# Optimization experiments

Measured on AMD Instinct MI355X. Metric: run time of the kernel, lower is better.

Reference implementation:

```python
import jax, jax.numpy as jnp
import numpy as np

N, E = 50000, 400000
F, P = 20, 8          # NUM_FREQ, NUM_POWER_CLASS (edge/node attn dim)
D, H = 128, 8         # d_model, heads
C = D // H            # head dim
FF, L = 512, 2        # dim_feedforward, num layers
EPS = 1e-5


def setup_inputs() -> dict:
    key = jax.random.key(0)
    ks = jax.random.split(key, 24)
    g = lambda k, s: jax.random.normal(k, s, dtype=jnp.float32) * 0.02
    return {
        "freq_alloc": jax.random.normal(ks[0], (N, F), jnp.float32),
        "node_power_attn": jax.random.normal(ks[1], (N, P), jnp.float32),
        "edge_power_attn": jax.random.normal(ks[2], (E, P), jnp.float32),
        "edge_index": jax.random.randint(ks[3], (2, E), 0, N),
        "ptr": jnp.sort(jax.random.randint(ks[4], (65,), 0, N)),
        # GraphTransformer input/embedding projections
        "W_in": g(ks[5], (F, D)), "b_in": jnp.zeros((D,), jnp.float32),
        "W_emb": g(ks[6], (P, D)), "b_emb": jnp.zeros((D,), jnp.float32),
        # per-layer TransformerConv params (stacked over L)
        "Wq": g(ks[7], (L, D, D)), "bq": jnp.zeros((L, D), jnp.float32),
        "Wk": g(ks[8], (L, D, D)), "bk": jnp.zeros((L, D), jnp.float32),
        "Wv": g(ks[9], (L, D, D)), "bv": jnp.zeros((L, D), jnp.float32),
        "We": g(ks[10], (L, P, D)),                      # lin_edge, bias=False
        "Wskip": g(ks[11], (L, D, D)), "bskip": jnp.zeros((L, D), jnp.float32),
        # per-layer FFN + LayerNorms
        "W1": g(ks[12], (L, D, FF)), "b1": jnp.zeros((L, FF), jnp.float32),
        "W2": g(ks[13], (L, FF, D)), "b2": jnp.zeros((L, D), jnp.float32),
        "ln1_g": jnp.ones((L, D), jnp.float32), "ln1_b": jnp.zeros((L, D), jnp.float32),
        "ln2_g": jnp.ones((L, D), jnp.float32), "ln2_b": jnp.zeros((L, D), jnp.float32),
        # output head
        "W_out": g(ks[14], (D, F)), "b_out": jnp.zeros((F,), jnp.float32),
    }


def _ln(x, g, b):
    mu = jnp.mean(x, axis=-1, keepdims=True)
    var = jnp.mean(jnp.square(x - mu), axis=-1, keepdims=True)
    return (x - mu) * jax.lax.rsqrt(var + EPS) * g + b


def reference(freq_alloc, node_power_attn, edge_power_attn, edge_index, ptr,
              W_in, b_in, W_emb, b_emb,
              Wq, bq, Wk, bk, Wv, bv, We, Wskip, bskip,
              W1, b1, W2, b2, ln1_g, ln1_b, ln2_g, ln2_b,
              W_out, b_out):
    # dropout layers are identity (inference / dropout=0)
    src, dst = edge_index[0], edge_index[1]  # PyG: messages flow src -> dst
    inp = freq_alloc @ W_in + b_in           # [N, D]
    x = node_power_attn @ W_emb + b_emb      # [N, D]
    scale = jnp.float32(1.0 / np.sqrt(C))
    for l in range(L):
        x = x + inp
        # --- TransformerConv (heads concat, root_weight=True, beta=False) ---
        q = (x @ Wq[l] + bq[l]).reshape(N, H, C)
        k = (x @ Wk[l] + bk[l]).reshape(N, H, C)
        v = (x @ Wv[l] + bv[l]).reshape(N, H, C)
        e = (edge_power_attn @ We[l]).reshape(E, H, C)   # edge embedding
        kj = k[src] + e                                   # [E, H, C]
        alpha = jnp.einsum('ehc,ehc->eh', q[dst], kj) * scale  # [E, H]
        # segment softmax over incoming edges of each dst node
        m = jnp.full((N, H), -jnp.inf, alpha.dtype).at[dst].max(alpha)
        ex = jnp.exp(alpha - m[dst])
        s = jnp.zeros((N, H), alpha.dtype).at[dst].add(ex)
        a = ex / s[dst]                                   # [E, H]
        msg = (v[src] + e) * a[:, :, None]                # [E, H, C]
        agg = jnp.zeros((N, H, C), x.dtype).at[dst].add(msg).reshape(N, D)
        x2 = agg + x @ Wskip[l] + bskip[l]
        # --- residual + norm + FFN + norm ---
        x = _ln(x + x2, ln1_g[l], ln1_b[l])
        x2 = jax.nn.relu(x @ W1[l] + b1[l]) @ W2[l] + b2[l]
        x = _ln(x + x2, ln2_g[l], ln2_b[l])
    logit = x @ W_out + b_out                             # [N, F]
    unallocated = jnp.sum(freq_alloc, axis=1, keepdims=True) < 1.0
    return jnp.where(unallocated, logit, -jnp.inf)
```

## Files before the change

### kernel.cpp

```cpp
#include <hip/hip_runtime.h>
#include <cstdint>
#include <cstddef>

typedef unsigned int uint;
typedef unsigned short ushort;
typedef unsigned char uchar;
typedef __attribute__((ext_vector_type(8))) short bf16x8;
typedef __attribute__((ext_vector_type(8))) ushort u16x8;
typedef __attribute__((ext_vector_type(4))) float f32x4;
typedef __attribute__((ext_vector_type(2))) float f32x2;
typedef __attribute__((ext_vector_type(2))) _Float16 h2v;

__device__ __forceinline__ ushort f2bf(float x) {
    uint u = __float_as_uint(x);
    u += 0x7fffu + ((u >> 16) & 1u);
    return (ushort)(u >> 16);
}
__device__ __forceinline__ float bflo(uint w) { return __uint_as_float(w << 16); }
__device__ __forceinline__ float bfhi(uint w) { return __uint_as_float(w & 0xffff0000u); }
__device__ __forceinline__ float bf1(ushort u) { return __uint_as_float(((uint)u) << 16); }
__device__ __forceinline__ uint pack2(float a, float b) { return (uint)f2bf(a) | ((uint)f2bf(b) << 16); }
__device__ __forceinline__ uint pack2h(float a, float b) {
    union { _Float16 h[2]; uint u; } c;
    c.h[0] = (_Float16)a; c.h[1] = (_Float16)b; return c.u;
}
__device__ __forceinline__ h2v ash2(uint u) { union { uint u; h2v h; } c; c.u = u; return c.h; }

__device__ __forceinline__ uchar enc8_sw(float x) {
    uint u = __float_as_uint(x);
    uint s = (u >> 31) << 7;
    float a = fabsf(x);
    if (a > 448.f) return (uchar)(s | 0x7E);
    if (a < 0.001953125f) return (uchar)s;
    int e; float m = frexpf(a, &e);
    int E = e - 1 + 7;
    if (E <= 0) {
        int qi = (int)(a * 512.f + 0.5f);
        if (qi > 7) qi = 7;
        return (uchar)(s | qi);
    }
    int M = (int)((m * 2.f - 1.f) * 8.f + 0.5f);
    if (M == 8) { M = 0; E++; }
    if (E > 15) return (uchar)(s | 0x7E);
    return (uchar)(s | (E << 3) | M);
}
__device__ __forceinline__ float dec8_sw(uint b) {
    int s = (b >> 7) & 1, E = (b >> 3) & 15, M = b & 7;
    float v = E ? ldexpf(1.f + M * 0.125f, E - 7) : ldexpf((float)M * 0.125f, -6);
    return s ? -v : v;
}
__device__ __forceinline__ uint pk8(float a, float b, float c, float d) {
#if __has_builtin(__builtin_amdgcn_cvt_pk_fp8_f32)
    int w = __builtin_amdgcn_cvt_pk_fp8_f32(a, b, 0, false);
    w = __builtin_amdgcn_cvt_pk_fp8_f32(c, d, w, true);
    return (uint)w;
#else
    return (uint)enc8_sw(a) | ((uint)enc8_sw(b) << 8) | ((uint)enc8_sw(c) << 16) | ((uint)enc8_sw(d) << 24);
#endif
}
__device__ __forceinline__ void dec4(uint w, float* o) {
#if __has_builtin(__builtin_amdgcn_cvt_pk_f32_fp8)
    f32x2 lo = __builtin_amdgcn_cvt_pk_f32_fp8(w, false);
    f32x2 hi = __builtin_amdgcn_cvt_pk_f32_fp8(w, true);
    o[0] = lo[0]; o[1] = lo[1]; o[2] = hi[0]; o[3] = hi[1];
#else
    o[0] = dec8_sw(w & 255); o[1] = dec8_sw((w >> 8) & 255);
    o[2] = dec8_sw((w >> 16) & 255); o[3] = dec8_sw((w >> 24) & 255);
#endif
}


__global__ __launch_bounds__(256) void k_zero_i(int* __restrict__ p, int n) {
    int i = blockIdx.x * 256 + threadIdx.x;
    if (i < n) p[i] = 0;
}

__global__ __launch_bounds__(256) void k_count(const int* __restrict__ dst, int* __restrict__ cnt, int n) {
    int i = blockIdx.x * 256 + threadIdx.x;
    if (i < n) atomicAdd(&cnt[dst[i]], 1);
}

__global__ __launch_bounds__(256) void k_scan1(const int* __restrict__ cnt, int* __restrict__ tmp,
                                               int* __restrict__ bsums, int n) {
    __shared__ int sc[256];
    int t = threadIdx.x;
    int base = blockIdx.x * 1024 + t * 4;
    int v0 = (base + 0 < n) ? cnt[base + 0] : 0;
    int v1 = (base + 1 < n) ? cnt[base + 1] : 0;
    int v2 = (base + 2 < n) ? cnt[base + 2] : 0;
    int v3 = (base + 3 < n) ? cnt[base + 3] : 0;
    int s = v0 + v1 + v2 + v3;
    sc[t] = s;
    __syncthreads();
    for (int off = 1; off < 256; off <<= 1) {
        int u = (t >= off) ? sc[t - off] : 0;
        __syncthreads();
        sc[t] += u;
        __syncthreads();
    }
    int excl = sc[t] - s;
    int r0 = excl + v0, r1 = r0 + v1, r2 = r1 + v2, r3 = r2 + v3;
    if (base + 0 < n) tmp[base + 0] = r0;
    if (base + 1 < n) tmp[base + 1] = r1;
    if (base + 2 < n) tmp[base + 2] = r2;
    if (base + 3 < n) tmp[base + 3] = r3;
    if (t == 255) bsums[blockIdx.x] = sc[255];
}

__global__ void k_scan2(int* __restrict__ bsums, int nb) {
    int l = threadIdx.x;
    int v = (l < nb) ? bsums[l] : 0;
    int incl = v;
    for (int off = 1; off < 64; off <<= 1) {
        int u = __shfl_up(incl, off);
        if (l >= off) incl += u;
    }
    if (l < nb) bsums[l] = incl - v;
}

__global__ __launch_bounds__(256) void k_scan3(const int* __restrict__ tmp, const int* __restrict__ bsums,
                                               int* __restrict__ rowptr, int n) {
    int t = threadIdx.x;
    int base = blockIdx.x * 1024 + t * 4;
    int off = bsums[blockIdx.x];
    #pragma unroll
    for (int i = 0; i < 4; i++) {
        int g = base + i;
        if (g < n) rowptr[g + 1] = tmp[g] + off;
    }
    if (blockIdx.x == 0 && t == 0) rowptr[0] = 0;
}

__global__ __launch_bounds__(256) void k_fill(
    const int* __restrict__ src, const int* __restrict__ dst,
    const int* __restrict__ rowptr, int* __restrict__ cur,
    const float* __restrict__ epa,
    int* __restrict__ srcp, ushort* __restrict__ epap, int n) {
    int e = blockIdx.x * 256 + threadIdx.x;
    if (e < n) {
        int d = dst[e];
        int pos = atomicAdd(&cur[d], 1);
        int slot = rowptr[d] + pos;
        srcp[slot] = src[e];
        float4 a = *(const float4*)(epa + (size_t)e * 8);
        float4 b = *(const float4*)(epa + (size_t)e * 8 + 4);
        u16x8 u;
        u[0] = f2bf(a.x); u[1] = f2bf(a.y); u[2] = f2bf(a.z); u[3] = f2bf(a.w);
        u[4] = f2bf(b.x); u[5] = f2bf(b.y); u[6] = f2bf(b.z); u[7] = f2bf(b.w);
        *(u16x8*)(epap + (size_t)slot * 8) = u;
    }
}

__global__ __launch_bounds__(256) void k_prep(
    const float* __restrict__ Wq, const float* __restrict__ Wk,
    const float* __restrict__ Wv, const float* __restrict__ Ws,
    const float* __restrict__ W1, const float* __restrict__ W2,
    ushort* __restrict__ qkvsT, ushort* __restrict__ W1T, ushort* __restrict__ W2T) {
    int tid = blockIdx.x * 256 + threadIdx.x;
    int l = tid / 196608;
    int r = tid % 196608;
    if (r < 65536) {
        int which = r >> 14, e = r & 16383;
        int k = e >> 7, c = e & 127;
        const float* s = (which == 0) ? Wq : (which == 1) ? Wk : (which == 2) ? Wv : Ws;
        qkvsT[(size_t)l * 81920 + (which * 128 + c) * 128 + k] = f2bf(s[l * 16384 + e]);
    } else if (r < 131072) {
        int e = r - 65536;
        int k = e >> 9, c = e & 511;
        W1T[l * 65536 + c * 128 + k] = f2bf(W1[l * 65536 + e]);
    } else {
        int e = r - 131072;
        int k = e >> 7, c = e & 127;
        W2T[l * 65536 + c * 512 + k] = f2bf(W2[l * 65536 + e]);
    }
}

__global__ __launch_bounds__(256) void k_prepqe(
    const float* __restrict__ Wq, const float* __restrict__ We, const float* __restrict__ bq,
    ushort* __restrict__ qkvsT, float* __restrict__ bqe) {
    int tid = blockIdx.x * 256 + threadIdx.x;
    int l = tid / 16512, r = tid % 16512;
    if (l > 1) return;
    ushort* base = qkvsT + (size_t)l * 81920;
    if (r < 8192) {
        int hp = r >> 7, i = r & 127;
        int h = hp >> 3, p = hp & 7;
        const float* wq = Wq + (size_t)l * 16384 + i * 128 + h * 16;
        const float* we = We + (size_t)l * 1024 + p * 128 + h * 16;
        float acc = 0.f;
        #pragma unroll
        for (int c = 0; c < 16; c++) acc += wq[c] * we[c];
        base[(512 + hp) * 128 + i] = f2bf(acc);
    } else if (r < 16384) {
        int z = r - 8192;
        base[(576 + (z >> 7)) * 128 + (z & 127)] = 0;
    } else {
        int j = r - 16384;
        float v = 0.f;
        if (j < 64) {
            int h = j >> 3, p = j & 7;
            #pragma unroll
            for (int c = 0; c < 16; c++)
                v += bq[l * 128 + h * 16 + c] * We[(size_t)l * 1024 + p * 128 + h * 16 + c];
        }
        bqe[l * 128 + j] = v;
    }
}

__global__ __launch_bounds__(256) void k_prepa(
    const float* __restrict__ fa, const float* __restrict__ npa,
    ushort* __restrict__ Ab, int n) {
    int tid = blockIdx.x * 256 + threadIdx.x;
    int node = tid >> 5, j = tid & 31;
    if (node >= n) return;
    float v;
    if (j < 20)      v = fa[(size_t)node * 20 + j];
    else if (j < 28) v = npa[(size_t)node * 8 + (j - 20)];
    else             v = (j == 28) ? 1.0f : 0.f;
    Ab[tid] = f2bf(v);
}

__global__ __launch_bounds__(256) void k_prepw(
    const float* __restrict__ Win, const float* __restrict__ bin,
    const float* __restrict__ Wemb, const float* __restrict__ bemb,
    ushort* __restrict__ BtIO) {
    int tid = blockIdx.x * 256 + threadIdx.x;
    if (tid >= 8192) return;
    int col = tid >> 5, k = tid & 31;
    int c = col & 127;
    float v = 0.f;
    if (k < 20) v = Win[k * 128 + c];
    else if (col >= 128 && k < 28) v = Wemb[(k - 20) * 128 + c];
    else if (k == 28) v = (col < 128) ? bin[c] : (bin[c] + bemb[c]);
    BtIO[tid] = f2bf(v);
}

__global__ __launch_bounds__(256) void k_inproj2(
    const ushort* __restrict__ Ab, const ushort* __restrict__ Bt,
    ushort* __restrict__ inpb, ushort* __restrict__ xib, int M) {
    __shared__ char As[8192];
    __shared__ char Bs[16384];
    int t = threadIdx.x, lane = t & 63, w = t >> 6;
    int wr = w >> 1, wc = w & 1;
    int l15 = lane & 15, l4 = lane >> 4;
    int rbase = blockIdx.x * 128;

    #pragma unroll
    for (int p = 0; p < 2; p++) {
        int idx = p * 256 + t;
        int row = idx >> 2, c8 = idx & 3;
        int grow = rbase + row;
        uint4 v = make_uint4(0u, 0u, 0u, 0u);
        if (grow < M) v = *(const uint4*)(Ab + (size_t)grow * 32 + c8 * 8);
        *(uint4*)(As + ((row * 64 + c8 * 16) ^ ((row & 7) << 4))) = v;
    }
    #pragma unroll
    for (int p = 0; p < 4; p++) {
        int idx = p * 256 + t;
        int col = idx >> 2, c8 = idx & 3;
        uint4 v = *(const uint4*)(Bt + (size_t)col * 32 + c8 * 8);
        *(uint4*)(Bs + ((col * 64 + c8 * 16) ^ ((col & 7) << 4))) = v;
    }
    __syncthreads();

    bf16x8 a[4], b[8];
    #pragma unroll
    for (int m = 0; m < 4; m++) {
        int row = wr * 64 + m * 16 + l15;
        a[m] = *(const bf16x8*)(As + ((row * 64 + l4 * 16) ^ ((row & 7) << 4)));
    }
    #pragma unroll
    for (int nn = 0; nn < 8; nn++) {
        int col = wc * 128 + nn * 16 + l15;
        b[nn] = *(const bf16x8*)(Bs + ((col * 64 + l4 * 16) ^ ((col & 7) << 4)));
    }
    f32x4 acc[4][8] = {};
    #pragma unroll
    for (int m = 0; m < 4; m++)
        #pragma unroll
        for (int nn = 0; nn < 8; nn++)
            acc[m][nn] = __builtin_amdgcn_mfma_f32_16x16x32_bf16(b[nn], a[m], acc[m][nn], 0, 0, 0);

    ushort* outp = wc ? xib : inpb;
    #pragma unroll
    for (int nn = 0; nn < 8; nn++) {
        int c0 = nn * 16 + l4 * 4;
        #pragma unroll
        for (int m = 0; m < 4; m++) {
            int grow = rbase + wr * 64 + m * 16 + l15;
            if (grow >= M) continue;
            uint2 pk = make_uint2(pack2(acc[m][nn][0], acc[m][nn][1]),
                                  pack2(acc[m][nn][2], acc[m][nn][3]));
            *(uint2*)(outp + (size_t)grow * 128 + c0) = pk;
        }
    }
}

struct OutDesc5 {
    ushort* bptr[5];
    uchar* p8[5];
    const float* bias[5];
    int bld[5];
    int wid[5];
    int mode[5];
    const ushort* res;
    int resbx;
};

__global__ __launch_bounds__(256) void k_qkvs_gemm(
    const ushort* __restrict__ A,
    const ushort* __restrict__ Bt,
    OutDesc5 od, int M) {
    __shared__ char smem[32768];
    char* As = smem;
    char* Bs = smem + 16384;
    int t = threadIdx.x;
    int lane = t & 63, w = t >> 6;
    int wr = w >> 1, wc = w & 1;
    int l15 = lane & 15, l4 = lane >> 4;
    int nwg = gridDim.x;
    int id = blockIdx.x;
    int q8 = nwg >> 3, r8 = nwg & 7;
    int xcd = id & 7, pos = id >> 3;
    int logical = (xcd < r8 ? xcd * (q8 + 1) : r8 * (q8 + 1) + (xcd - r8) * q8) + pos;
    int bx = logical % 5;
    int rbase = (logical / 5) * 128;
    int cbase = bx * 128;

    f32x4 acc[4][4] = {};

    for (int kb = 0; kb < 128; kb += 64) {
        #pragma unroll
        for (int p = 0; p < 4; p++) {
            int idx = p * 256 + t;
            int row = idx >> 3, c8 = idx & 7;
            int grow = rbase + row;
            uint4 v = make_uint4(0u, 0u, 0u, 0u);
            if (grow < M) v = *(const uint4*)(A + (size_t)grow * 128 + kb + c8 * 8);
            *(uint4*)(As + ((row * 128 + c8 * 16) ^ ((row & 7) << 4))) = v;
        }
        #pragma unroll
        for (int p = 0; p < 4; p++) {
            int idx = p * 256 + t;
            int col = idx >> 3, c8 = idx & 7;
            uint4 v = *(const uint4*)(Bt + (size_t)(cbase + col) * 128 + kb + c8 * 8);
            *(uint4*)(Bs + ((col * 128 + c8 * 16) ^ ((col & 7) << 4))) = v;
        }
        __syncthreads();
        #pragma unroll
        for (int kk = 0; kk < 2; kk++) {
            int kbyte = kk * 64 + l4 * 16;
            bf16x8 a[4], b[4];
            #pragma unroll
            for (int m = 0; m < 4; m++) {
                int row = wr * 64 + m * 16 + l15;
                a[m] = *(const bf16x8*)(As + ((row * 128 + kbyte) ^ ((row & 7) << 4)));
            }
            #pragma unroll
            for (int nn = 0; nn < 4; nn++) {
                int col = wc * 64 + nn * 16 + l15;
                b[nn] = *(const bf16x8*)(Bs + ((col * 128 + kbyte) ^ ((col & 7) << 4)));
            }
            #pragma unroll
            for (int m = 0; m < 4; m++)
                #pragma unroll
                for (int nn = 0; nn < 4; nn++)
                    acc[m][nn] = __builtin_amdgcn_mfma_f32_16x16x32_bf16(b[nn], a[m], acc[m][nn], 0, 0, 0);
        }
        __syncthreads();
    }

    int wid = od.wid[bx];
    const float* bias = od.bias[bx];
    int bld = od.bld[bx];
    int mode = od.mode[bx];
    bool addres = (bx == od.resbx);
    #pragma unroll
    for (int nn = 0; nn < 4; nn++) {
        int c0 = wc * 64 + nn * 16 + l4 * 4;
        if (c0 >= wid) continue;
        float4 b4 = *(const float4*)(bias + c0);
        #pragma unroll
        for (int m = 0; m < 4; m++) {
            int grow = rbase + wr * 64 + m * 16 + l15;
            if (grow >= M) continue;
            float v0 = acc[m][nn][0] + b4.x;
            float v1 = acc[m][nn][1] + b4.y;
            float v2 = acc[m][nn][2] + b4.z;
            float v3 = acc[m][nn][3] + b4.w;
            if (addres) {
                uint2 rv = *(const uint2*)(od.res + (size_t)grow * 128 + c0);
                v0 += bflo(rv.x); v1 += bfhi(rv.x);
                v2 += bflo(rv.y); v3 += bfhi(rv.y);
            }
            if (mode == 2) {
                *(uint*)(od.p8[bx] + (size_t)grow * bld + c0) = pk8(v0, v1, v2, v3);
            } else {
                uint2 pk;
                if (mode == 1) pk = make_uint2(pack2h(v0, v1), pack2h(v2, v3));
                else           pk = make_uint2(pack2(v0, v1), pack2(v2, v3));
                *(uint2*)(od.bptr[bx] + (size_t)grow * bld + c0) = pk;
            }
        }
    }
}

template <bool ADDINP>
__global__ __launch_bounds__(512) void k_ffn(
    const ushort* __restrict__ h1b,
    const ushort* __restrict__ W1T,
    const ushort* __restrict__ W2T,
    const float* __restrict__ b1, const float* __restrict__ b2,
    const float* __restrict__ g, const float* __restrict__ bb,
    const ushort* __restrict__ inpb,
    ushort* __restrict__ xib, int M) {
    __shared__ char As[32768];
    __shared__ char Wsb[16384];
    __shared__ char Hs[128 * 136];
    int t = threadIdx.x, lane = t & 63, w = t >> 6;
    int rbase = blockIdx.x * 128;
    int l15 = lane & 15, l4 = lane >> 4;
    int rowhalf = (w >> 2) * 64;
    int icol = (w & 3) * 16 + l15;

    #pragma unroll
    for (int p = 0; p < 4; p++) {
        int idx = p * 512 + t;
        int row = idx >> 4, c8 = idx & 15;
        int grow = rbase + row;
        uint4 v = make_uint4(0u, 0u, 0u, 0u);
        if (grow < M) v = *(const uint4*)(h1b + (size_t)grow * 128 + c8 * 8);
        *(uint4*)(As + ((row * 256 + c8 * 16) ^ ((row & 7) << 4))) = v;
    }

    const ushort* w1base = W1T + (size_t)icol * 128;
    bf16x8 wfn[4];
    #pragma unroll
    for (int kk = 0; kk < 4; kk++)
        wfn[kk] = *(const bf16x8*)(w1base + kk * 32 + l4 * 8);

    f32x4 acco[8] = {};
    __syncthreads();

    for (int ch = 0; ch < 8; ch++) {
        uint4 w2r[2];
        #pragma unroll
        for (int p = 0; p < 2; p++) {
            int idx = p * 512 + t;
            int oc = idx >> 3, c8 = idx & 7;
            w2r[p] = *(const uint4*)(W2T + (size_t)oc * 512 + ch * 64 + c8 * 8);
        }
        bf16x8 wfc[4];
        #pragma unroll
        for (int kk = 0; kk < 4; kk++) wfc[kk] = wfn[kk];
        if (ch < 7) {
            const ushort* nb = w1base + (size_t)(ch + 1) * 8192;
            #pragma unroll
            for (int kk = 0; kk < 4; kk++)
                wfn[kk] = *(const bf16x8*)(nb + kk * 32 + l4 * 8);
        }
        f32x4 acch[4] = {};
        #pragma unroll
        for (int kk = 0; kk < 4; kk++) {
            int kbyte = kk * 64 + l4 * 16;
            #pragma unroll
            for (int j = 0; j < 4; j++) {
                int row = rowhalf + j * 16 + l15;
                bf16x8 hf = *(const bf16x8*)(As + ((row * 256 + kbyte) ^ ((row & 7) << 4)));
                acch[j] = __builtin_amdgcn_mfma_f32_16x16x32_bf16(wfc[kk], hf, acch[j], 0, 0, 0);
            }
        }
        {
            int hc0 = (w & 3) * 16 + l4 * 4;
            float4 b1v = *(const float4*)(b1 + ch * 64 + hc0);
            #pragma unroll
            for (int j = 0; j < 4; j++) {
                int row = rowhalf + j * 16 + l15;
                float v0 = fmaxf(acch[j][0] + b1v.x, 0.f);
                float v1 = fmaxf(acch[j][1] + b1v.y, 0.f);
                float v2 = fmaxf(acch[j][2] + b1v.z, 0.f);
                float v3 = fmaxf(acch[j][3] + b1v.w, 0.f);
                uint2 pk = make_uint2(pack2(v0, v1), pack2(v2, v3));
                *(uint2*)(Hs + row * 136 + hc0 * 2) = pk;
            }
        }
        #pragma unroll
        for (int p = 0; p < 2; p++) {
            int idx = p * 512 + t;
            int oc = idx >> 3, c8 = idx & 7;
            *(uint4*)(Wsb + ((oc * 128 + c8 * 16) ^ ((oc & 7) << 4))) = w2r[p];
        }
        __syncthreads();
        #pragma unroll
        for (int kk = 0; kk < 2; kk++) {
            int kbyte = kk * 64 + l4 * 16;
            bf16x8 a = *(const bf16x8*)(Hs + (w * 16 + l15) * 136 + kbyte);
            #pragma unroll
            for (int nn = 0; nn < 8; nn++) {
                int oc = nn * 16 + l15;
                bf16x8 b = *(const bf16x8*)(Wsb + ((oc * 128 + kbyte) ^ ((oc & 7) << 4)));
                acco[nn] = __builtin_amdgcn_mfma_f32_16x16x32_bf16(a, b, acco[nn], 0, 0, 0);
            }
        }
        __syncthreads();
    }

    float b2v[8], gg[8], bbv[8];
    #pragma unroll
    for (int nn = 0; nn < 8; nn++) {
        int coll = nn * 16 + l15;
        b2v[nn] = b2[coll]; gg[nn] = g[coll]; bbv[nn] = bb[coll];
    }
    #pragma unroll
    for (int r = 0; r < 4; r++) {
        int rowt = w * 16 + l4 * 4 + r;
        int grow = rbase + rowt;
        float pre[8];
        float s1 = 0.f, s2 = 0.f;
        #pragma unroll
        for (int nn = 0; nn < 8; nn++) {
            int coll = nn * 16 + l15;
            float rv = bf1(*(const ushort*)(As + ((rowt * 256 + coll * 2) ^ ((rowt & 7) << 4))));
            float v = acco[nn][r] + b2v[nn] + rv;
            pre[nn] = v;
            s1 += v; s2 += v * v;
        }
        #pragma unroll
        for (int mask = 1; mask <= 8; mask <<= 1) {
            s1 += __shfl_xor(s1, mask);
            s2 += __shfl_xor(s2, mask);
        }
        float mu = s1 * (1.f / 128.f);
        float var = s2 * (1.f / 128.f) - mu * mu;
        float rsq = rsqrtf(var + 1e-5f);
        if (grow < M) {
            #pragma unroll
            for (int nn = 0; nn < 8; nn++) {
                int coll = nn * 16 + l15;
                float v = (pre[nn] - mu) * rsq * gg[nn] + bbv[nn];
                if (ADDINP) v += bf1(inpb[(size_t)grow * 128 + coll]);
                xib[(size_t)grow * 128 + coll] = f2bf(v);
            }
        }
    }
}

__global__ __launch_bounds__(256) void k_attn(
    const ushort* __restrict__ qsb, const uchar* __restrict__ kv8,
    const ushort* __restrict__ qeb,
    const int* __restrict__ srcp, const ushort* __restrict__ epap,
    const int* __restrict__ rowptr,
    const float* __restrict__ We,
    const float* __restrict__ g1, const float* __restrict__ be1,
    ushort* __restrict__ h1, int n) {
    int wave = threadIdx.x >> 6, lane = threadIdx.x & 63;
    int nhalf = lane >> 5, l32 = lane & 31;
    int s = l32 >> 3, h = l32 & 7;
    int node = blockIdx.x * 8 + wave * 2 + nhalf;
    if (node >= n) node = n - 1;
    int d0 = h * 16 + s * 4;
    const ushort* qrow = qsb + (size_t)node * 256;
    uint4 qh0 = *(const uint4*)(qrow + h * 16);
    uint4 qh1 = *(const uint4*)(qrow + h * 16 + 8);
    uint2 sw = *(const uint2*)(qrow + 128 + d0);
    uint4 qe = *(const uint4*)(qeb + (size_t)node * 64 + h * 8);
    int beg = rowptr[node];
    int end = rowptr[node + 1];
    float4 gv = *(const float4*)(g1 + d0);
    float4 bv = *(const float4*)(be1 + d0);

    float qf[16];
    {
        h2v p;
        p = ash2(qh0.x); qf[0] = p[0]; qf[1] = p[1];
        p = ash2(qh0.y); qf[2] = p[0]; qf[3] = p[1];
        p = ash2(qh0.z); qf[4] = p[0]; qf[5] = p[1];
        p = ash2(qh0.w); qf[6] = p[0]; qf[7] = p[1];
        p = ash2(qh1.x); qf[8] = p[0]; qf[9] = p[1];
        p = ash2(qh1.y); qf[10] = p[0]; qf[11] = p[1];
        p = ash2(qh1.z); qf[12] = p[0]; qf[13] = p[1];
        p = ash2(qh1.w); qf[14] = p[0]; qf[15] = p[1];
    }
    float qe8[8];
    qe8[0] = bflo(qe.x); qe8[1] = bfhi(qe.x); qe8[2] = bflo(qe.y); qe8[3] = bfhi(qe.y);
    qe8[4] = bflo(qe.z); qe8[5] = bfhi(qe.z); qe8[6] = bflo(qe.w); qe8[7] = bfhi(qe.w);

    float sacc = 0.f, va[16], awp[8];
    #pragma unroll
    for (int c = 0; c < 16; c++) va[c] = 0.f;
    #pragma unroll
    for (int p = 0; p < 8; p++) awp[p] = 0.f;

    for (int base = beg; base < end; base += 4) {
        int i = base + s;
        bool ve = i < end;
        int ii = ve ? i : beg;
        int sn = srcp[ii];
        uint4 ew = *(const uint4*)(epap + (size_t)ii * 8);
        const uchar* kr = kv8 + (size_t)sn * 256 + h * 16;
        uint4 kw = *(const uint4*)(kr);
        uint4 vw = *(const uint4*)(kr + 128);
        float ep[8];
        ep[0] = bflo(ew.x); ep[1] = bfhi(ew.x); ep[2] = bflo(ew.y); ep[3] = bfhi(ew.y);
        ep[4] = bflo(ew.z); ep[5] = bfhi(ew.z); ep[6] = bflo(ew.w); ep[7] = bfhi(ew.w);
        float kf[16];
        dec4(kw.x, kf); dec4(kw.y, kf + 4); dec4(kw.z, kf + 8); dec4(kw.w, kf + 12);
        float dt = 0.f;
        #pragma unroll
        for (int c = 0; c < 16; c++) dt += qf[c] * kf[c];
        #pragma unroll
        for (int p = 0; p < 8; p++) dt += qe8[p] * ep[p];
        float ex = ve ? __expf(dt * 0.25f) : 0.f;
        sacc += ex;
        float vf[16];
        dec4(vw.x, vf); dec4(vw.y, vf + 4); dec4(vw.z, vf + 8); dec4(vw.w, vf + 12);
        #pragma unroll
        for (int c = 0; c < 16; c++) va[c] += ex * vf[c];
        #pragma unroll
        for (int p = 0; p < 8; p++) awp[p] += ex * ep[p];
    }

    float v8[8];
    bool hiA = (s & 2) != 0;
    #pragma unroll
    for (int j = 0; j < 8; j++) {
        float keep = hiA ? va[8 + j] : va[j];
        float send = hiA ? va[j] : va[8 + j];
        v8[j] = keep + __shfl_xor(send, 16);
    }
    float v4[4];
    bool hiB = (s & 1) != 0;
    #pragma unroll
    for (int j = 0; j < 4; j++) {
        float keep = hiB ? v8[4 + j] : v8[j];
        float send = hiB ? v8[j] : v8[4 + j];
        v4[j] = keep + __shfl_xor(send, 8);
    }
    #pragma unroll
    for (int mask = 8; mask <= 16; mask <<= 1) {
        sacc += __shfl_xor(sacc, mask);
        #pragma unroll
        for (int p = 0; p < 8; p++) awp[p] += __shfl_xor(awp[p], mask);
    }

    float agg[4];
    {
        float4 we4[8];
        #pragma unroll
        for (int p = 0; p < 8; p++) we4[p] = *(const float4*)(We + p * 128 + d0);
        #pragma unroll
        for (int j = 0; j < 4; j++) {
            float a = v4[j];
            #pragma unroll
            for (int p = 0; p < 8; p++) a += awp[p] * ((const float*)&we4[p])[j];
            agg[j] = a;
        }
    }
    float invs = (end > beg) ? 1.f / sacc : 0.f;

    float pre[4];
    pre[0] = agg[0] * invs + bflo(sw.x);
    pre[1] = agg[1] * invs + bfhi(sw.x);
    pre[2] = agg[2] * invs + bflo(sw.y);
    pre[3] = agg[3] * invs + bfhi(sw.y);
    float s1 = pre[0] + pre[1] + pre[2] + pre[3];
    float s2 = pre[0] * pre[0] + pre[1] * pre[1] + pre[2] * pre[2] + pre[3] * pre[3];
    #pragma unroll
    for (int off = 1; off <= 16; off <<= 1) {
        s1 += __shfl_xor(s1, off);
        s2 += __shfl_xor(s2, off);
    }
    float mu = s1 * (1.f / 128.f);
    float var = s2 * (1.f / 128.f) - mu * mu;
    float rs = rsqrtf(var + 1e-5f);
    float o0 = (pre[0] - mu) * rs * gv.x + bv.x;
    float o1 = (pre[1] - mu) * rs * gv.y + bv.y;
    float o2 = (pre[2] - mu) * rs * gv.z + bv.z;
    float o3 = (pre[3] - mu) * rs * gv.w + bv.w;
    uint2 pk = make_uint2(pack2(o0, o1), pack2(o2, o3));
    *(uint2*)(h1 + (size_t)node * 128 + d0) = pk;
}

__global__ __launch_bounds__(256) void k_out(
    const ushort* __restrict__ x, const float* __restrict__ Wout, const float* __restrict__ bout,
    const float* __restrict__ fa, float* __restrict__ out, int n) {
    __shared__ float xs[8][128];
    __shared__ float ws[128][20];
    __shared__ float bs[20];
    int t = threadIdx.x;
    int nodeBase = blockIdx.x * 8;
    for (int i = t; i < 2560; i += 256) ws[i / 20][i % 20] = Wout[i];
    if (t < 20) bs[t] = bout[t];
    {
        int row = t >> 5, c4 = t & 31;
        int node = nodeBase + row;
        int nc = node < n ? node : (n - 1);
        uint2 v = *(const uint2*)(x + (size_t)nc * 128 + c4 * 4);
        xs[row][c4 * 4 + 0] = bflo(v.x); xs[row][c4 * 4 + 1] = bfhi(v.x);
        xs[row][c4 * 4 + 2] = bflo(v.y); xs[row][c4 * 4 + 3] = bfhi(v.y);
    }
    int row = t >> 5, jj = t & 31;
    int node = nodeBase + row;
    bool vn = node < n;
    float fv = (vn && jj < 20) ? fa[(size_t)node * 20 + jj] : 0.f;
    float rsum = fv;
    #pragma unroll
    for (int m = 16; m >= 1; m >>= 1) rsum += __shfl_xor(rsum, m);
    __syncthreads();
    if (!vn || jj >= 20) return;
    float acc = bs[jj];
    #pragma unroll 16
    for (int d = 0; d < 128; d++) acc += xs[row][d] * ws[d][jj];
    out[(size_t)node * 20 + jj] = (rsum < 1.0f) ? acc : -3.0e38f;
}

extern "C" void kernel_launch(void* const* d_in, const int* in_sizes, int n_in,
                              void* d_out, int out_size, void* d_ws, size_t ws_size,
                              hipStream_t stream) {
    const float* fa    = (const float*)d_in[0];
    const float* npa   = (const float*)d_in[1];
    const float* epa   = (const float*)d_in[2];
    const int*   ei    = (const int*)d_in[3];
    const float* Win   = (const float*)d_in[5];
    const float* bin   = (const float*)d_in[6];
    const float* Wemb  = (const float*)d_in[7];
    const float* bemb  = (const float*)d_in[8];
    const float* Wq    = (const float*)d_in[9];
    const float* bqv   = (const float*)d_in[10];
    const float* Wk    = (const float*)d_in[11];
    const float* bkv   = (const float*)d_in[12];
    const float* Wv    = (const float*)d_in[13];
    const float* bvv   = (const float*)d_in[14];
    const float* We    = (const float*)d_in[15];
    const float* Wskip = (const float*)d_in[16];
    const float* bskip = (const float*)d_in[17];
    const float* W1    = (const float*)d_in[18];
    const float* b1    = (const float*)d_in[19];
    const float* W2    = (const float*)d_in[20];
    const float* b2    = (const float*)d_in[21];
    const float* ln1g  = (const float*)d_in[22];
    const float* ln1b  = (const float*)d_in[23];
    const float* ln2g  = (const float*)d_in[24];
    const float* ln2b  = (const float*)d_in[25];
    const float* Wout  = (const float*)d_in[26];
    const float* bout  = (const float*)d_in[27];

    const int N = in_sizes[0] / 20;
    const int E = in_sizes[2] / 8;

    char* wp = (char*)d_ws;
    #define WS_ALLOC(ty, name, count) ty* name = (ty*)wp; wp += (((size_t)(count) * sizeof(ty)) + 63) & ~(size_t)63;
    WS_ALLOC(ushort, xib,  (size_t)N * 128)
    WS_ALLOC(ushort, h1b,  (size_t)N * 128)
    WS_ALLOC(ushort, inpb, (size_t)N * 128)
    WS_ALLOC(ushort, qsb,  (size_t)N * 256)
    WS_ALLOC(uchar,  kv8,  (size_t)N * 256)
    WS_ALLOC(ushort, qeb,  (size_t)N * 64)
    WS_ALLOC(ushort, Ab,   (size_t)N * 32)
    WS_ALLOC(ushort, qkvsT, 2 * 81920)
    WS_ALLOC(ushort, W1T,   2 * 65536)
    WS_ALLOC(ushort, W2T,   2 * 65536)
    WS_ALLOC(ushort, BtIO,  8192)
    WS_ALLOC(float,  bqe,   256)
    WS_ALLOC(ushort, epap,  (size_t)E * 8)
    WS_ALLOC(int,    srcp,  E)
    WS_ALLOC(int,    rowptr, N + 1)
    WS_ALLOC(int,    cnt,    N)
    WS_ALLOC(int,    cur,    N)
    WS_ALLOC(int,    tmp,    N)
    WS_ALLOC(int,    bsums,  64)
    #undef WS_ALLOC

    const int* srcs = ei;
    const int* dsts = ei + E;

    k_zero_i<<<(2 * N + 255) / 256, 256, 0, stream>>>(cnt, 2 * N);
    k_count<<<(E + 255) / 256, 256, 0, stream>>>(dsts, cnt, E);
    int nb = (N + 1023) / 1024;
    k_scan1<<<nb, 256, 0, stream>>>(cnt, tmp, bsums, N);
    k_scan2<<<1, 64, 0, stream>>>(bsums, nb);
    k_scan3<<<nb, 256, 0, stream>>>(tmp, bsums, rowptr, N);
    k_fill<<<(E + 255) / 256, 256, 0, stream>>>(srcs, dsts, rowptr, cur, epa, srcp, epap, E);

    k_prep<<<1536, 256, 0, stream>>>(Wq, Wk, Wv, Wskip, W1, W2, qkvsT, W1T, W2T);
    k_prepqe<<<130, 256, 0, stream>>>(Wq, We, bqv, qkvsT, bqe);
    k_prepw<<<32, 256, 0, stream>>>(Win, bin, Wemb, bemb, BtIO);
    k_prepa<<<((size_t)N * 32 + 255) / 256, 256, 0, stream>>>(fa, npa, Ab, N);

    int qblocks = (N + 127) / 128;
    int fblocks = (N + 127) / 128;

    k_inproj2<<<qblocks, 256, 0, stream>>>(Ab, BtIO, inpb, xib, N);

    for (int l = 0; l < 2; l++) {
        {
            OutDesc5 od = {};
            od.bptr[0] = qsb;        od.bias[0] = bqv + l * 128;   od.bld[0] = 256; od.wid[0] = 128; od.mode[0] = 1;
            od.p8[1]   = kv8;        od.bias[1] = bkv + l * 128;   od.bld[1] = 256; od.wid[1] = 128; od.mode[1] = 2;
            od.p8[2]   = kv8 + 128;  od.bias[2] = bvv + l * 128;   od.bld[2] = 256; od.wid[2] = 128; od.mode[2] = 2;
            od.bptr[3] = qsb + 128;  od.bias[3] = bskip + l * 128; od.bld[3] = 256; od.wid[3] = 128; od.mode[3] = 0;
            od.bptr[4] = qeb;        od.bias[4] = bqe + l * 128;   od.bld[4] = 64;  od.wid[4] = 64;  od.mode[4] = 0;
            od.res = xib; od.resbx = 3;
            k_qkvs_gemm<<<5 * qblocks, 256, 0, stream>>>(
                xib, qkvsT + (size_t)l * 81920, od, N);
        }

        k_attn<<<(N + 7) / 8, 256, 0, stream>>>(qsb, kv8, qeb, srcp, epap, rowptr,
                                                We + (size_t)l * 1024,
                                                ln1g + l * 128, ln1b + l * 128, h1b, N);

        if (l == 0)
            k_ffn<true><<<fblocks, 512, 0, stream>>>(
                h1b, W1T, W2T, b1, b2, ln2g, ln2b, inpb, xib, N);
        else
            k_ffn<false><<<fblocks, 512, 0, stream>>>(
                h1b, W1T + 65536, W2T + 65536, b1 + 512, b2 + 128,
                ln2g + 128, ln2b + 128, nullptr, xib, N);
    }

    k_out<<<(N + 7) / 8, 256, 0, stream>>>(xib, Wout, bout, fa, (float*)d_out, N);
}
```

Before: 308.0 us.

## Prefetch next GEMM K-tile into registers and double-buffer edge gathers

The GEMM K loop is unrolled so the second 64-wide A tile is loaded into registers while the MFMAs on the first tile run. The edge-attention loop now keeps the next two groups of edge gathers (src index, edge attr, K/V rows) in registers, so memory latency overlaps with the dot product and accumulation. The cost is more live registers, which may lower occupancy.

Result: no change. 305.4 us (-0.8%).

```diff
diff --git a/kernel.cpp b/kernel.cpp
--- a/kernel.cpp
+++ b/kernel.cpp
@@ -329,45 +329,90 @@
 
     f32x4 acc[4][4] = {};
 
-    for (int kb = 0; kb < 128; kb += 64) {
-        #pragma unroll
-        for (int p = 0; p < 4; p++) {
-            int idx = p * 256 + t;
-            int row = idx >> 3, c8 = idx & 7;
-            int grow = rbase + row;
-            uint4 v = make_uint4(0u, 0u, 0u, 0u);
-            if (grow < M) v = *(const uint4*)(A + (size_t)grow * 128 + kb + c8 * 8);
-            *(uint4*)(As + ((row * 128 + c8 * 16) ^ ((row & 7) << 4))) = v;
-        }
-        #pragma unroll
-        for (int p = 0; p < 4; p++) {
-            int idx = p * 256 + t;
-            int col = idx >> 3, c8 = idx & 7;
-            uint4 v = *(const uint4*)(Bt + (size_t)(cbase + col) * 128 + kb + c8 * 8);
-            *(uint4*)(Bs + ((col * 128 + c8 * 16) ^ ((col & 7) << 4))) = v;
-        }
-        __syncthreads();
-        #pragma unroll
-        for (int kk = 0; kk < 2; kk++) {
-            int kbyte = kk * 64 + l4 * 16;
-            bf16x8 a[4], b[4];
+    #pragma unroll
+    for (int p = 0; p < 4; p++) {
+        int idx = p * 256 + t;
+        int row = idx >> 3, c8 = idx & 7;
+        int grow = rbase + row;
+        uint4 v = make_uint4(0u, 0u, 0u, 0u);
+        if (grow < M) v = *(const uint4*)(A + (size_t)grow * 128 + c8 * 8);
+        *(uint4*)(As + ((row * 128 + c8 * 16) ^ ((row & 7) << 4))) = v;
+    }
+    #pragma unroll
+    for (int p = 0; p < 4; p++) {
+        int idx = p * 256 + t;
+        int col = idx >> 3, c8 = idx & 7;
+        uint4 v = *(const uint4*)(Bt + (size_t)(cbase + col) * 128 + c8 * 8);
+        *(uint4*)(Bs + ((col * 128 + c8 * 16) ^ ((col & 7) << 4))) = v;
+    }
+    __syncthreads();
+
+    uint4 apre[4];
+    #pragma unroll
+    for (int p = 0; p < 4; p++) {
+        int idx = p * 256 + t;
+        int row = idx >> 3, c8 = idx & 7;
+        int grow = rbase + row;
+        apre[p] = make_uint4(0u, 0u, 0u, 0u);
+        if (grow < M) apre[p] = *(const uint4*)(A + (size_t)grow * 128 + 64 + c8 * 8);
+    }
+
+    #pragma unroll
+    for (int kk = 0; kk < 2; kk++) {
+        int kbyte = kk * 64 + l4 * 16;
+        bf16x8 a[4], b[4];
+        #pragma unroll
+        for (int m = 0; m < 4; m++) {
+            int row = wr * 64 + m * 16 + l15;
+            a[m] = *(const bf16x8*)(As + ((row * 128 + kbyte) ^ ((row & 7) << 4)));
+        }
+        #pragma unroll
+        for (int nn = 0; nn < 4; nn++) {
+            int col = wc * 64 + nn * 16 + l15;
+            b[nn] = *(const bf16x8*)(Bs + ((col * 128 + kbyte) ^ ((col & 7) << 4)));
+        }
+        #pragma unroll
+        for (int m = 0; m < 4; m++)
             #pragma unroll
-            for (int m = 0; m < 4; m++) {
-                int row = wr * 64 + m * 16 + l15;
-                a[m] = *(const bf16x8*)(As + ((row * 128 + kbyte) ^ ((row & 7) << 4)));
-            }
+            for (int nn = 0; nn < 4; nn++)
+                acc[m][nn] = __builtin_amdgcn_mfma_f32_16x16x32_bf16(b[nn], a[m], acc[m][nn], 0, 0, 0);
+    }
+    __syncthreads();
+
+    #pragma unroll
+    for (int p = 0; p < 4; p++) {
+        int idx = p * 256 + t;
+        int row = idx >> 3, c8 = idx & 7;
+        *(uint4*)(As + ((row * 128 + c8 * 16) ^ ((row & 7) << 4))) = apre[p];
+    }
+    #pragma unroll
+    for (int p = 0; p < 4; p++) {
+        int idx = p * 256 + t;
+        int col = idx >> 3, c8 = idx & 7;
+        uint4 v = *(const uint4*)(Bt + (size_t)(cbase + col) * 128 + 64 + c8 * 8);
+        *(uint4*)(Bs + ((col * 128 + c8 * 16) ^ ((col & 7) << 4))) = v;
+    }
+    __syncthreads();
+
+    #pragma unroll
+    for (int kk = 0; kk < 2; kk++) {
+        int kbyte = kk * 64 + l4 * 16;
+        bf16x8 a[4], b[4];
+        #pragma unroll
+        for (int m = 0; m < 4; m++) {
+            int row = wr * 64 + m * 16 + l15;
+            a[m] = *(const bf16x8*)(As + ((row * 128 + kbyte) ^ ((row & 7) << 4)));
+        }
+        #pragma unroll
+        for (int nn = 0; nn < 4; nn++) {
+            int col = wc * 64 + nn * 16 + l15;
+            b[nn] = *(const bf16x8*)(Bs + ((col * 128 + kbyte) ^ ((col & 7) << 4)));
+        }
+        #pragma unroll
+        for (int m = 0; m < 4; m++)
             #pragma unroll
-            for (int nn = 0; nn < 4; nn++) {
-                int col = wc * 64 + nn * 16 + l15;
-                b[nn] = *(const bf16x8*)(Bs + ((col * 128 + kbyte) ^ ((col & 7) << 4)));
-            }
-            #pragma unroll
-            for (int m = 0; m < 4; m++)
-                #pragma unroll
-                for (int nn = 0; nn < 4; nn++)
-                    acc[m][nn] = __builtin_amdgcn_mfma_f32_16x16x32_bf16(b[nn], a[m], acc[m][nn], 0, 0, 0);
-        }
-        __syncthreads();
+            for (int nn = 0; nn < 4; nn++)
+                acc[m][nn] = __builtin_amdgcn_mfma_f32_16x16x32_bf16(b[nn], a[m], acc[m][nn], 0, 0, 0);
     }
 
     int wid = od.wid[bx];
@@ -591,15 +636,47 @@
     #pragma unroll
     for (int p = 0; p < 8; p++) awp[p] = 0.f;
 
+    bool ve0 = false, ve1 = false;
+    uint4 ew0 = make_uint4(0u, 0u, 0u, 0u), kw0 = ew0, vw0 = ew0;
+    uint4 ew1 = ew0, kw1 = ew0, vw1 = ew0;
+    if (beg < end) {
+        int i = beg + s;
+        ve0 = i < end;
+        int ii = ve0 ? i : beg;
+        int sn = srcp[ii];
+        ew0 = *(const uint4*)(epap + (size_t)ii * 8);
+        const uchar* kr = kv8 + (size_t)sn * 256 + h * 16;
+        kw0 = *(const uint4*)(kr);
+        vw0 = *(const uint4*)(kr + 128);
+    }
+    if (beg + 4 < end) {
+        int i = beg + 4 + s;
+        ve1 = i < end;
+        int ii = ve1 ? i : beg;
+        int sn = srcp[ii];
+        ew1 = *(const uint4*)(epap + (size_t)ii * 8);
+        const uchar* kr = kv8 + (size_t)sn * 256 + h * 16;
+        kw1 = *(const uint4*)(kr);
+        vw1 = *(const uint4*)(kr + 128);
+    }
+
     for (int base = beg; base < end; base += 4) {
-        int i = base + s;
-        bool ve = i < end;
-        int ii = ve ? i : beg;
-        int sn = srcp[ii];
-        uint4 ew = *(const uint4*)(epap + (size_t)ii * 8);
-        const uchar* kr = kv8 + (size_t)sn * 256 + h * 16;
-        uint4 kw = *(const uint4*)(kr);
-        uint4 vw = *(const uint4*)(kr + 128);
+        bool ve = ve0;
+        uint4 ew = ew0, kw = kw0, vw = vw0;
+        ve0 = ve1; ew0 = ew1; kw0 = kw1; vw0 = vw1;
+        int nb2 = base + 8;
+        if (nb2 < end) {
+            int i = nb2 + s;
+            ve1 = i < end;
+            int ii = ve1 ? i : beg;
+            int sn = srcp[ii];
+            ew1 = *(const uint4*)(epap + (size_t)ii * 8);
+            const uchar* kr = kv8 + (size_t)sn * 256 + h * 16;
+            kw1 = *(const uint4*)(kr);
+            vw1 = *(const uint4*)(kr + 128);
+        } else {
+            ve1 = false;
+        }
         float ep[8];
         ep[0] = bflo(ew.x); ep[1] = bfhi(ew.x); ep[2] = bflo(ew.y); ep[3] = bfhi(ew.y);
         ep[4] = bflo(ew.z); ep[5] = bfhi(ew.z); ep[6] = bflo(ew.w); ep[7] = bfhi(ew.w);
```
